# Kernel optimization log

Hardware: AMD Instinct MI355X
Metric: run time of the kernel (lower is better)

The kernel has to match this reference:

```python
import jax, jax.numpy as jnp
import numpy as np

B, S, D, P, N_IMGS = 64, 197, 768, 196, 50000  # S = P + 1 (class token)
GRID = float(np.sqrt(P))  # 14.0, matches np.sqrt(no_of_patches)


def setup_inputs() -> dict:
    key = jax.random.key(0)
    ks = jax.random.split(key, 12)
    x = jax.random.normal(ks[0], (B, S, D), dtype=jnp.float32)
    img_ids = jax.random.randint(ks[1], (B,), 0, N_IMGS, dtype=jnp.int32)
    mask = jnp.zeros((B, S), dtype=jnp.bool_)  # unused by the module's forward
    w = 0.02
    Wq = w * jax.random.normal(ks[2], (D, D), dtype=jnp.float32)
    bq = jnp.zeros((D,), dtype=jnp.float32)
    Wk = w * jax.random.normal(ks[3], (D, D), dtype=jnp.float32)
    bk = jnp.zeros((D,), dtype=jnp.float32)
    Wv = w * jax.random.normal(ks[4], (D, D), dtype=jnp.float32)
    bv = jnp.zeros((D,), dtype=jnp.float32)
    # per-image Gaussian params (init: avgs~0, std_devs=1 as in the module)
    avgs = 0.05 * jax.random.normal(ks[5], (N_IMGS, 2, P), dtype=jnp.float32)
    std_devs = jnp.ones((N_IMGS, 2, P), dtype=jnp.float32)
    # the torch code draws fresh N(0,1) noise per image inside forward; we
    # materialize it as an input for determinism: noise[:,0]=norm_x, noise[:,1]=norm_y
    noise = jax.random.normal(ks[6], (B, 2, P), dtype=jnp.float32)
    return {"x": x, "img_ids": img_ids, "mask": mask, "Wq": Wq, "bq": bq,
            "Wk": Wk, "bk": bk, "Wv": Wv, "bv": bv,
            "avgs": avgs, "std_devs": std_devs, "noise": noise}


def _gather(t, idx):
    # t: (B,S,D), idx: (B,P) -> (B,P,D)
    return jnp.take_along_axis(t, idx[:, :, None], axis=1)


def reference(x, img_ids, mask, Wq, bq, Wk, bk, Wv, bv, avgs, std_devs, noise):
    q = x @ Wq + bq
    k = x @ Wk + bk
    v = x @ Wv + bv

    a = avgs[img_ids]        # (B,2,P)
    s = std_devs[img_ids]    # (B,2,P)
    key_x = (noise[:, 0] - a[:, 0]) / s[:, 0]  # (B,P)
    key_y = (noise[:, 1] - a[:, 1]) / s[:, 1]

    x1, x2 = jnp.ceil(key_x), jnp.floor(key_x)
    y1, y2 = jnp.ceil(key_y), jnp.floor(key_y)

    def bilin(px, py):  # (1-|px-kx|)*(1-|py-ky|)
        return (1.0 - jnp.abs(px - key_x)) * (1.0 - jnp.abs(py - key_y))

    def idx(px, py):  # long-cast (truncation) of grid*y+x, wrapped like torch neg-indexing
        return (GRID * py + px).astype(jnp.int32) % S

    w11, w21, w12, w22 = bilin(x1, y1), bilin(x2, y1), bilin(x1, y2), bilin(x2, y2)
    i11, i21, i12, i22 = idx(x1, y1), idx(x2, y1), idx(x1, y2), idx(x2, y2)

    def sample(t):  # bilinear 4-point gather -> (B,P,D)
        return (w11[:, :, None] * _gather(t, i11)
                + w21[:, :, None] * _gather(t, i21)
                + w12[:, :, None] * _gather(t, i12)
                + w22[:, :, None] * _gather(t, i22))

    sk = sample(k)
    sv = sample(v)

    cls = jnp.ones((x.shape[0], 1, D), dtype=x.dtype)  # class_emb = ones(1,1,D)
    sk = jnp.concatenate([cls, sk], axis=1)  # (B,S,D)
    sv = jnp.concatenate([cls, sv], axis=1)  # (B,S,D)

    # at_sc[b,s] = <sampled_key[b,s], q[b,s]>; original shape (S,1,1) per image,
    # softmax over the singleton dim (faithful to F.softmax(at_sc, dim=1))
    scores = jnp.einsum('bsd,bsd->bs', sk, q)[:, :, None]  # (B,S,1)
    attn = jax.nn.softmax(scores, axis=-1)                 # ones (singleton axis)
    out = attn * sv                                        # (B,S,D)
    return out
```

## Files before the change

kernel.cpp:

```cpp
#include <hip/hip_runtime.h>
#include <cstdint>
#include <cstddef>

#define Bb 64
#define Ss 197
#define Dd 768
#define Pp 196

typedef short bf16x8 __attribute__((ext_vector_type(8)));
typedef short bf16x4 __attribute__((ext_vector_type(4)));
typedef float f32x4  __attribute__((ext_vector_type(4)));
struct alignas(16) F4 { float v[4]; };

__device__ __forceinline__ int mod_s(int v) {
    int r = v % Ss;
    return (r < 0) ? r + Ss : r;
}

__device__ __forceinline__ unsigned short f2bf(float f) {
    union { float f; unsigned u; } v; v.f = f;
    unsigned r = (v.u + 0x7FFFu + ((v.u >> 16) & 1u)) >> 16;
    return (unsigned short)r;
}

__device__ __forceinline__ void gload_lds16(const void* g, void* l) {
    __builtin_amdgcn_global_load_lds(
        (const __attribute__((address_space(1))) unsigned int*)g,
        (__attribute__((address_space(3))) unsigned int*)l, 16, 0, 0);
}

struct GParams {
    float w0, w1, w2, w3;
    int i0, i1, i2, i3;
};

__device__ __forceinline__ GParams gather_params(
    const int* img_ids, const float* avgs, const float* stds,
    const float* noise, int b, int p)
{
    const int id = img_ids[b];
    const float a0 = avgs [((size_t)id * 2    ) * Pp + p];
    const float a1 = avgs [((size_t)id * 2 + 1) * Pp + p];
    const float s0 = stds [((size_t)id * 2    ) * Pp + p];
    const float s1 = stds [((size_t)id * 2 + 1) * Pp + p];
    const float nx = noise[((size_t)b  * 2    ) * Pp + p];
    const float ny = noise[((size_t)b  * 2 + 1) * Pp + p];
    const float kx = (nx - a0) / s0;
    const float ky = (ny - a1) / s1;
    const float cx = ceilf(kx),  fx = floorf(kx);
    const float cy = ceilf(ky),  fy = floorf(ky);
    const float dcx = 1.0f - fabsf(cx - kx);
    const float dfx = 1.0f - fabsf(fx - kx);
    const float dcy = 1.0f - fabsf(cy - ky);
    const float dfy = 1.0f - fabsf(fy - ky);
    GParams g;
    g.w0 = dcx * dcy;  g.w1 = dfx * dcy;  g.w2 = dcx * dfy;  g.w3 = dfx * dfy;
    g.i0 = mod_s((int)(14.0f * cy + cx));
    g.i1 = mod_s((int)(14.0f * cy + fx));
    g.i2 = mod_s((int)(14.0f * fy + cx));
    g.i3 = mod_s((int)(14.0f * fy + fx));
    return g;
}

#define GATHER_BLKS 3328
#define TRANS_BLKS  144

__global__ __launch_bounds__(256) void gsa_prep(
    const float* __restrict__ x,
    const int*   __restrict__ img_ids,
    const float* __restrict__ Wv,
    const float* __restrict__ avgs,
    const float* __restrict__ stds,
    const float* __restrict__ noise,
    unsigned short* __restrict__ Ag,
    unsigned short* __restrict__ WvT,
    float* __restrict__ wsB,
    float* __restrict__ out)
{
    __shared__ short T[64][66];
    const int t   = threadIdx.x;
    const int blk = blockIdx.x;

    if (blk < GATHER_BLKS) {
        const int xcd  = blk & 7;
        const int s    = blk >> 3;
        const int tl   = s >> 5;
        const int r    = s & 31;
        const int tile = tl * 8 + xcd;
        if (tile < 98) {
            const int lane = t & 63;
            const int w    = t >> 6;
            const int m    = tile * 128 + r * 4 + w;
            const int b    = m / Pp;
            const int p    = m - b * Pp;
            GParams g = gather_params(img_ids, avgs, stds, noise, b, p);
            const size_t xb = (size_t)b * Ss;
            const float* r0 = x + (xb + g.i0) * Dd;
            const float* r1 = x + (xb + g.i1) * Dd;
            const float* r2 = x + (xb + g.i2) * Dd;
            const float* r3 = x + (xb + g.i3) * Dd;
            unsigned short* dst = Ag + (size_t)m * Dd;
            #pragma unroll
            for (int c = 0; c < 3; ++c) {
                const int k = c * 256 + lane * 4;
                F4 v0 = *reinterpret_cast<const F4*>(r0 + k);
                F4 v1 = *reinterpret_cast<const F4*>(r1 + k);
                F4 v2 = *reinterpret_cast<const F4*>(r2 + k);
                F4 v3 = *reinterpret_cast<const F4*>(r3 + k);
                bf16x4 o;
                #pragma unroll
                for (int q = 0; q < 4; ++q)
                    o[q] = (short)f2bf(g.w0*v0.v[q] + g.w1*v1.v[q] + g.w2*v2.v[q] + g.w3*v3.v[q]);
                *reinterpret_cast<bf16x4*>(dst + k) = o;
            }
            if (lane == 0) wsB[m] = g.w0 + g.w1 + g.w2 + g.w3;
        } else {
            const int cb  = (xcd - 2) * 32 + r;
            const int idx = cb * 256 + t;
            const int b = idx / Dd;
            const int d = idx - b * Dd;
            out[(size_t)b * Ss * Dd + d] = 1.0f;
        }
    } else {
        const int tb = blk - GATHER_BLKS;
        const int k0 = (tb % 12) * 64;
        const int n0 = (tb / 12) * 64;
        const int tx = t & 63, tyy = t >> 6;
        #pragma unroll
        for (int pass = 0; pass < 16; ++pass) {
            const int i = pass * 4 + tyy;
            T[i][tx] = (short)f2bf(Wv[(size_t)(k0 + i) * Dd + n0 + tx]);
        }
        __syncthreads();
        #pragma unroll
        for (int pass = 0; pass < 16; ++pass) {
            const int n = pass * 4 + tyy;
            WvT[(size_t)(n0 + n) * Dd + k0 + tx] = (unsigned short)T[tx][n];
        }
    }
}

#define NSTG 12

__global__ __launch_bounds__(256, 6) void gsa_gemm5(
    const unsigned short* __restrict__ Ag,
    const unsigned short* __restrict__ WvT,
    const float* __restrict__ wsB,
    const float* __restrict__ bv,
    float* __restrict__ out)
{
    __shared__ short lds[12288];

    const int t = threadIdx.x;
    const int L      = blockIdx.x;
    const int xcd    = L & 7;
    const int grp    = L >> 3;
    const int n_t    = grp % 6;
    const int mchunk = grp / 6;
    const int m_tile = mchunk * 8 + xcd;
    if (m_tile >= 196) return;
    const int m0 = m_tile * 64;
    const int n0 = n_t * 128;

    const int lane = t & 63;
    const int w    = t >> 6;

    const unsigned short* aSrc[2];
    const unsigned short* bSrc[4];
    int ldsA[2], ldsB[4];
    #pragma unroll
    for (int i = 0; i < 2; ++i) {
        const int rr = (w * 2 + i) * 8 + (lane >> 3);
        const int qq = (lane & 7) ^ (rr & 7);
        aSrc[i] = Ag + (size_t)(m0 + rr) * Dd + qq * 8;
        ldsA[i] = (w * 2 + i) * 512;
    }
    #pragma unroll
    for (int i = 0; i < 4; ++i) {
        const int rr = (w * 4 + i) * 8 + (lane >> 3);
        const int qq = (lane & 7) ^ (rr & 7);
        bSrc[i] = WvT + (size_t)(n0 + rr) * Dd + qq * 8;
        ldsB[i] = 4096 + (w * 4 + i) * 512;
    }

    const int col  = lane & 15;
    const int quad = lane >> 4;
    const int wm   = (w & 1) * 32;
    const int wn   = (w >> 1) * 64;
    int offA[2][2], offB[4][2];
    #pragma unroll
    for (int i = 0; i < 2; ++i) {
        const int ra = wm + i * 16 + col;
        #pragma unroll
        for (int ks = 0; ks < 2; ++ks)
            offA[i][ks] = (ra * 8 + ((ks * 4 + quad) ^ (ra & 7))) * 8;
    }
    #pragma unroll
    for (int i = 0; i < 4; ++i) {
        const int rb = wn + i * 16 + col;
        #pragma unroll
        for (int ks = 0; ks < 2; ++ks)
            offB[i][ks] = 4096 + (rb * 8 + ((ks * 4 + quad) ^ (rb & 7))) * 8;
    }

    f32x4 acc[2][4];
    #pragma unroll
    for (int i = 0; i < 2; ++i)
        #pragma unroll
        for (int j = 0; j < 4; ++j) acc[i][j] = (f32x4)0.0f;

    for (int s = 0; s < NSTG; ++s) {
        const int kadv = s * 64;
        if (s > 0) __syncthreads();
        #pragma unroll
        for (int i = 0; i < 2; ++i) gload_lds16(aSrc[i] + kadv, &lds[ldsA[i]]);
        #pragma unroll
        for (int i = 0; i < 4; ++i) gload_lds16(bSrc[i] + kadv, &lds[ldsB[i]]);
        __syncthreads();
        #pragma unroll
        for (int ks = 0; ks < 2; ++ks) {
            bf16x8 aF[2], bF[4];
            #pragma unroll
            for (int mi = 0; mi < 2; ++mi)
                aF[mi] = *reinterpret_cast<const bf16x8*>(lds + offA[mi][ks]);
            #pragma unroll
            for (int ni = 0; ni < 4; ++ni)
                bF[ni] = *reinterpret_cast<const bf16x8*>(lds + offB[ni][ks]);
            #pragma unroll
            for (int mi = 0; mi < 2; ++mi)
                #pragma unroll
                for (int ni = 0; ni < 4; ++ni)
                    acc[mi][ni] = __builtin_amdgcn_mfma_f32_16x16x32_bf16(
                        aF[mi], bF[ni], acc[mi][ni], 0, 0, 0);
        }
    }

    float bvv[4];
    #pragma unroll
    for (int ni = 0; ni < 4; ++ni) bvv[ni] = bv[n0 + wn + ni * 16 + col];

    #pragma unroll
    for (int mi = 0; mi < 2; ++mi) {
        #pragma unroll
        for (int rg = 0; rg < 4; ++rg) {
            const int mg = m0 + wm + mi * 16 + quad * 4 + rg;
            const int b  = mg / Pp;
            const float wsv = wsB[mg];
            float* orow = out + ((size_t)(mg + b + 1)) * Dd;
            #pragma unroll
            for (int ni = 0; ni < 4; ++ni)
                orow[n0 + wn + ni * 16 + col] = acc[mi][ni][rg] + wsv * bvv[ni];
        }
    }
}

extern "C" void kernel_launch(void* const* d_in, const int* in_sizes, int n_in,
                              void* d_out, int out_size, void* d_ws, size_t ws_size,
                              hipStream_t stream) {
    const float* x       = (const float*)d_in[0];
    const int*   img_ids = (const int*)  d_in[1];
    const float* Wv      = (const float*)d_in[7];
    const float* bv      = (const float*)d_in[8];
    const float* avgs    = (const float*)d_in[9];
    const float* stds    = (const float*)d_in[10];
    const float* noise   = (const float*)d_in[11];
    float* out = (float*)d_out;

    const size_t ag_bytes  = (size_t)Bb * Pp * Dd * sizeof(unsigned short);
    const size_t wvt_bytes = (size_t)Dd * Dd * sizeof(unsigned short);
    unsigned short* Ag  = (unsigned short*)d_ws;
    unsigned short* WvT = (unsigned short*)((char*)d_ws + ag_bytes);
    float*          wsB = (float*)((char*)d_ws + ag_bytes + wvt_bytes);

    gsa_prep<<<GATHER_BLKS + TRANS_BLKS, 256, 0, stream>>>(
        x, img_ids, Wv, avgs, stds, noise, Ag, WvT, wsB, out);
    gsa_gemm5<<<1200, 256, 0, stream>>>(Ag, WvT, wsB, bv, out);
}
```

Before: 212.0 us.

## Fuse prep and GEMM into one persistent kernel with grid barrier

Merges the gather/transpose prep kernel and the bf16 MFMA GEMM into one persistent 1024-block kernel that synchronises through an atomic grid-wide barrier. Rows are assigned so that each XCD gathers the A rows it later consumes, and the transposed Wv is written once per XCD so B-tile loads stay in local L2. This removes a kernel launch and the gap between the two kernels. In exchange it adds a spin barrier that needs all blocks co-resident, a guard-based timeout that could break correctness, eight copies of Wv to write, and a workgroup-scope acquire fence that may not be strong enough across the device.

```diff
diff --git a/kernel.cpp b/kernel.cpp
--- a/kernel.cpp
+++ b/kernel.cpp
@@ -11,6 +11,8 @@
 typedef short bf16x4 __attribute__((ext_vector_type(4)));
 typedef float f32x4  __attribute__((ext_vector_type(4)));
 struct alignas(16) F4 { float v[4]; };
+
+__device__ unsigned long long g_bar;
 
 __device__ __forceinline__ int mod_s(int v) {
     int r = v % Ss;
@@ -62,126 +64,111 @@
     return g;
 }
 
-#define GATHER_BLKS 3328
-#define TRANS_BLKS  144
-
-__global__ __launch_bounds__(256) void gsa_prep(
+#define GRID_BLKS 1024
+#define NSTG 12
+
+__global__ __launch_bounds__(256, 4) void gsa_fused(
     const float* __restrict__ x,
     const int*   __restrict__ img_ids,
     const float* __restrict__ Wv,
     const float* __restrict__ avgs,
     const float* __restrict__ stds,
     const float* __restrict__ noise,
+    const float* __restrict__ bv,
     unsigned short* __restrict__ Ag,
-    unsigned short* __restrict__ WvT,
+    unsigned short* __restrict__ WvTrep,
     float* __restrict__ wsB,
     float* __restrict__ out)
 {
-    __shared__ short T[64][66];
-    const int t   = threadIdx.x;
-    const int blk = blockIdx.x;
-
-    if (blk < GATHER_BLKS) {
-        const int xcd  = blk & 7;
-        const int s    = blk >> 3;
-        const int tl   = s >> 5;
-        const int r    = s & 31;
-        const int tile = tl * 8 + xcd;
-        if (tile < 98) {
-            const int lane = t & 63;
-            const int w    = t >> 6;
-            const int m    = tile * 128 + r * 4 + w;
-            const int b    = m / Pp;
-            const int p    = m - b * Pp;
-            GParams g = gather_params(img_ids, avgs, stds, noise, b, p);
-            const size_t xb = (size_t)b * Ss;
-            const float* r0 = x + (xb + g.i0) * Dd;
-            const float* r1 = x + (xb + g.i1) * Dd;
-            const float* r2 = x + (xb + g.i2) * Dd;
-            const float* r3 = x + (xb + g.i3) * Dd;
-            unsigned short* dst = Ag + (size_t)m * Dd;
-            #pragma unroll
-            for (int c = 0; c < 3; ++c) {
-                const int k = c * 256 + lane * 4;
-                F4 v0 = *reinterpret_cast<const F4*>(r0 + k);
-                F4 v1 = *reinterpret_cast<const F4*>(r1 + k);
-                F4 v2 = *reinterpret_cast<const F4*>(r2 + k);
-                F4 v3 = *reinterpret_cast<const F4*>(r3 + k);
-                bf16x4 o;
-                #pragma unroll
-                for (int q = 0; q < 4; ++q)
-                    o[q] = (short)f2bf(g.w0*v0.v[q] + g.w1*v1.v[q] + g.w2*v2.v[q] + g.w3*v3.v[q]);
-                *reinterpret_cast<bf16x4*>(dst + k) = o;
-            }
-            if (lane == 0) wsB[m] = g.w0 + g.w1 + g.w2 + g.w3;
-        } else {
-            const int cb  = (xcd - 2) * 32 + r;
-            const int idx = cb * 256 + t;
-            const int b = idx / Dd;
-            const int d = idx - b * Dd;
-            out[(size_t)b * Ss * Dd + d] = 1.0f;
-        }
-    } else {
-        const int tb = blk - GATHER_BLKS;
-        const int k0 = (tb % 12) * 64;
-        const int n0 = (tb / 12) * 64;
-        const int tx = t & 63, tyy = t >> 6;
-        #pragma unroll
-        for (int pass = 0; pass < 16; ++pass) {
-            const int i = pass * 4 + tyy;
-            T[i][tx] = (short)f2bf(Wv[(size_t)(k0 + i) * Dd + n0 + tx]);
-        }
-        __syncthreads();
-        #pragma unroll
-        for (int pass = 0; pass < 16; ++pass) {
-            const int n = pass * 4 + tyy;
-            WvT[(size_t)(n0 + n) * Dd + k0 + tx] = (unsigned short)T[tx][n];
-        }
-    }
-}
-
-#define NSTG 12
-
-__global__ __launch_bounds__(256, 6) void gsa_gemm5(
-    const unsigned short* __restrict__ Ag,
-    const unsigned short* __restrict__ WvT,
-    const float* __restrict__ wsB,
-    const float* __restrict__ bv,
-    float* __restrict__ out)
-{
     __shared__ short lds[12288];
 
-    const int t = threadIdx.x;
-    const int L      = blockIdx.x;
-    const int xcd    = L & 7;
-    const int grp    = L >> 3;
-    const int n_t    = grp % 6;
-    const int mchunk = grp / 6;
-    const int m_tile = mchunk * 8 + xcd;
-    if (m_tile >= 196) return;
-    const int m0 = m_tile * 64;
-    const int n0 = n_t * 128;
-
+    const int t    = threadIdx.x;
+    const int bid  = blockIdx.x;
+    const int xcd  = bid & 7;
+    const int j    = bid >> 3;
     const int lane = t & 63;
     const int w    = t >> 6;
 
-    const unsigned short* aSrc[2];
-    const unsigned short* bSrc[4];
-    int ldsA[2], ldsB[4];
+    const int tilesM = (xcd < 4) ? 25 : 24;
+    const int rowsX  = tilesM * 64;
+
     #pragma unroll
-    for (int i = 0; i < 2; ++i) {
-        const int rr = (w * 2 + i) * 8 + (lane >> 3);
-        const int qq = (lane & 7) ^ (rr & 7);
-        aSrc[i] = Ag + (size_t)(m0 + rr) * Dd + qq * 8;
-        ldsA[i] = (w * 2 + i) * 512;
-    }
-    #pragma unroll
-    for (int i = 0; i < 4; ++i) {
-        const int rr = (w * 4 + i) * 8 + (lane >> 3);
-        const int qq = (lane & 7) ^ (rr & 7);
-        bSrc[i] = WvT + (size_t)(n0 + rr) * Dd + qq * 8;
-        ldsB[i] = 4096 + (w * 4 + i) * 512;
-    }
+    for (int sidx = 0; sidx < 4; ++sidx) {
+        const int s = w + sidx * 4;
+        if (s >= 13) continue;
+        const int r = j * 13 + s;
+        if (r >= rowsX) continue;
+        const int tile = (r >> 6) * 8 + xcd;
+        const int m    = tile * 64 + (r & 63);
+        const int b    = m / Pp;
+        const int p    = m - b * Pp;
+        GParams g = gather_params(img_ids, avgs, stds, noise, b, p);
+        const size_t xb = (size_t)b * Ss;
+        const float* r0 = x + (xb + g.i0) * Dd;
+        const float* r1 = x + (xb + g.i1) * Dd;
+        const float* r2 = x + (xb + g.i2) * Dd;
+        const float* r3 = x + (xb + g.i3) * Dd;
+        unsigned short* dst = Ag + (size_t)m * Dd;
+        #pragma unroll
+        for (int c = 0; c < 3; ++c) {
+            const int k = c * 256 + lane * 4;
+            F4 v0 = *reinterpret_cast<const F4*>(r0 + k);
+            F4 v1 = *reinterpret_cast<const F4*>(r1 + k);
+            F4 v2 = *reinterpret_cast<const F4*>(r2 + k);
+            F4 v3 = *reinterpret_cast<const F4*>(r3 + k);
+            bf16x4 o;
+            #pragma unroll
+            for (int q = 0; q < 4; ++q)
+                o[q] = (short)f2bf(g.w0*v0.v[q] + g.w1*v1.v[q] + g.w2*v2.v[q] + g.w3*v3.v[q]);
+            *reinterpret_cast<bf16x4*>(dst + k) = o;
+        }
+        if (lane == 0) wsB[m] = g.w0 + g.w1 + g.w2 + g.w3;
+    }
+
+    unsigned short* rep = WvTrep + (size_t)xcd * Dd * Dd;
+    {
+        short (*T)[66] = reinterpret_cast<short(*)[66]>(lds);
+        const int tx = t & 63, tyy = t >> 6;
+        for (int tt = j; tt < 144; tt += 128) {
+            const int k0 = (tt % 12) * 64;
+            const int n0 = (tt / 12) * 64;
+            __syncthreads();
+            #pragma unroll
+            for (int pass = 0; pass < 16; ++pass) {
+                const int i = pass * 4 + tyy;
+                T[i][tx] = (short)f2bf(Wv[(size_t)(k0 + i) * Dd + n0 + tx]);
+            }
+            __syncthreads();
+            #pragma unroll
+            for (int pass = 0; pass < 16; ++pass) {
+                const int n = pass * 4 + tyy;
+                rep[(size_t)(n0 + n) * Dd + k0 + tx] = (unsigned short)T[tx][n];
+            }
+        }
+    }
+
+    if (bid < 192) {
+        const int idx = bid * 256 + t;
+        const int b = idx / Dd;
+        const int d = idx - b * Dd;
+        out[(size_t)b * Ss * Dd + d] = 1.0f;
+    }
+
+    __syncthreads();
+    if (t == 0) {
+        const unsigned long long old =
+            __hip_atomic_fetch_add(&g_bar, 1ull, __ATOMIC_RELAXED,
+                                   __HIP_MEMORY_SCOPE_AGENT);
+        const unsigned long long target = (old / GRID_BLKS + 1ull) * GRID_BLKS;
+        int guard = 0;
+        while (__hip_atomic_load(&g_bar, __ATOMIC_RELAXED,
+                                 __HIP_MEMORY_SCOPE_AGENT) < target) {
+            __builtin_amdgcn_s_sleep(8);
+            if (++guard > 400000) break;
+        }
+    }
+    __syncthreads();
+    __builtin_amdgcn_fence(__ATOMIC_ACQUIRE, "workgroup");
 
     const int col  = lane & 15;
     const int quad = lane >> 4;
@@ -203,53 +190,79 @@
             offB[i][ks] = 4096 + (rb * 8 + ((ks * 4 + quad) ^ (rb & 7))) * 8;
     }
 
-    f32x4 acc[2][4];
-    #pragma unroll
-    for (int i = 0; i < 2; ++i)
-        #pragma unroll
-        for (int j = 0; j < 4; ++j) acc[i][j] = (f32x4)0.0f;
-
-    for (int s = 0; s < NSTG; ++s) {
-        const int kadv = s * 64;
-        if (s > 0) __syncthreads();
-        #pragma unroll
-        for (int i = 0; i < 2; ++i) gload_lds16(aSrc[i] + kadv, &lds[ldsA[i]]);
-        #pragma unroll
-        for (int i = 0; i < 4; ++i) gload_lds16(bSrc[i] + kadv, &lds[ldsB[i]]);
-        __syncthreads();
-        #pragma unroll
-        for (int ks = 0; ks < 2; ++ks) {
-            bf16x8 aF[2], bF[4];
-            #pragma unroll
-            for (int mi = 0; mi < 2; ++mi)
-                aF[mi] = *reinterpret_cast<const bf16x8*>(lds + offA[mi][ks]);
-            #pragma unroll
-            for (int ni = 0; ni < 4; ++ni)
-                bF[ni] = *reinterpret_cast<const bf16x8*>(lds + offB[ni][ks]);
-            #pragma unroll
-            for (int mi = 0; mi < 2; ++mi)
+    for (int u = j; u < tilesM * 6; u += 128) {
+        const int n_t    = u % 6;
+        const int mchunk = u / 6;
+        const int m_tile = mchunk * 8 + xcd;
+        const int m0 = m_tile * 64;
+        const int n0 = n_t * 128;
+
+        const unsigned short* aSrc[2];
+        const unsigned short* bSrc[4];
+        int ldsA[2], ldsB[4];
+        #pragma unroll
+        for (int i = 0; i < 2; ++i) {
+            const int rr = (w * 2 + i) * 8 + (lane >> 3);
+            const int qq = (lane & 7) ^ (rr & 7);
+            aSrc[i] = Ag + (size_t)(m0 + rr) * Dd + qq * 8;
+            ldsA[i] = (w * 2 + i) * 512;
+        }
+        #pragma unroll
+        for (int i = 0; i < 4; ++i) {
+            const int rr = (w * 4 + i) * 8 + (lane >> 3);
+            const int qq = (lane & 7) ^ (rr & 7);
+            bSrc[i] = rep + (size_t)(n0 + rr) * Dd + qq * 8;
+            ldsB[i] = 4096 + (w * 4 + i) * 512;
+        }
+
+        f32x4 acc[2][4];
+        #pragma unroll
+        for (int i = 0; i < 2; ++i)
+            #pragma unroll
+            for (int jj = 0; jj < 4; ++jj) acc[i][jj] = (f32x4)0.0f;
+
+        for (int s = 0; s < NSTG; ++s) {
+            const int kadv = s * 64;
+            __syncthreads();
+            #pragma unroll
+            for (int i = 0; i < 2; ++i) gload_lds16(aSrc[i] + kadv, &lds[ldsA[i]]);
+            #pragma unroll
+            for (int i = 0; i < 4; ++i) gload_lds16(bSrc[i] + kadv, &lds[ldsB[i]]);
+            __syncthreads();
+            #pragma unroll
+            for (int ks = 0; ks < 2; ++ks) {
+                bf16x8 aF[2], bF[4];
+                #pragma unroll
+                for (int mi = 0; mi < 2; ++mi)
+                    aF[mi] = *reinterpret_cast<const bf16x8*>(lds + offA[mi][ks]);
                 #pragma unroll
                 for (int ni = 0; ni < 4; ++ni)
-                    acc[mi][ni] = __builtin_amdgcn_mfma_f32_16x16x32_bf16(
-                        aF[mi], bF[ni], acc[mi][ni], 0, 0, 0);
-        }
-    }
-
-    float bvv[4];
-    #pragma unroll
-    for (int ni = 0; ni < 4; ++ni) bvv[ni] = bv[n0 + wn + ni * 16 + col];
-
-    #pragma unroll
-    for (int mi = 0; mi < 2; ++mi) {
-        #pragma unroll
-        for (int rg = 0; rg < 4; ++rg) {
-            const int mg = m0 + wm + mi * 16 + quad * 4 + rg;
-            const int b  = mg / Pp;
-            const float wsv = wsB[mg];
-            float* orow = out + ((size_t)(mg + b + 1)) * Dd;
-            #pragma unroll
-            for (int ni = 0; ni < 4; ++ni)
-                orow[n0 + wn + ni * 16 + col] = acc[mi][ni][rg] + wsv * bvv[ni];
+                    bF[ni] = *reinterpret_cast<const bf16x8*>(lds + offB[ni][ks]);
+                #pragma unroll
+                for (int mi = 0; mi < 2; ++mi)
+                    #pragma unroll
+                    for (int ni = 0; ni < 4; ++ni)
+                        acc[mi][ni] = __builtin_amdgcn_mfma_f32_16x16x32_bf16(
+                            aF[mi], bF[ni], acc[mi][ni], 0, 0, 0);
+            }
+        }
+
+        float bvv[4];
+        #pragma unroll
+        for (int ni = 0; ni < 4; ++ni) bvv[ni] = bv[n0 + wn + ni * 16 + col];
+
+        #pragma unroll
+        for (int mi = 0; mi < 2; ++mi) {
+            #pragma unroll
+            for (int rg = 0; rg < 4; ++rg) {
+                const int mg = m0 + wm + mi * 16 + quad * 4 + rg;
+                const int b  = mg / Pp;
+                const float wsv = wsB[mg];
+                float* orow = out + ((size_t)(mg + b + 1)) * Dd;
+                #pragma unroll
+                for (int ni = 0; ni < 4; ++ni)
+                    orow[n0 + wn + ni * 16 + col] = acc[mi][ni][rg] + wsv * bvv[ni];
+            }
         }
     }
 }
@@ -267,12 +280,11 @@
     float* out = (float*)d_out;
 
     const size_t ag_bytes  = (size_t)Bb * Pp * Dd * sizeof(unsigned short);
-    const size_t wvt_bytes = (size_t)Dd * Dd * sizeof(unsigned short);
-    unsigned short* Ag  = (unsigned short*)d_ws;
-    unsigned short* WvT = (unsigned short*)((char*)d_ws + ag_bytes);
-    float*          wsB = (float*)((char*)d_ws + ag_bytes + wvt_bytes);
-
-    gsa_prep<<<GATHER_BLKS + TRANS_BLKS, 256, 0, stream>>>(
-        x, img_ids, Wv, avgs, stds, noise, Ag, WvT, wsB, out);
-    gsa_gemm5<<<1200, 256, 0, stream>>>(Ag, WvT, wsB, bv, out);
-}
+    const size_t rep_bytes = (size_t)8 * Dd * Dd * sizeof(unsigned short);
+    unsigned short* Ag     = (unsigned short*)d_ws;
+    unsigned short* WvTrep = (unsigned short*)((char*)d_ws + ag_bytes);
+    float*          wsB    = (float*)((char*)d_ws + ag_bytes + rep_bytes);
+
+    gsa_fused<<<GRID_BLKS, 256, 0, stream>>>(
+        x, img_ids, Wv, avgs, stds, noise, bv, Ag, WvTrep, wsB, out);
+}
```

New measurement: 299.3 us. +41.2%, slower.
